# Performance work log

Measured on AMD Instinct MI355X. Metric: run time of the kernel, lower is better.

Reference implementation:

```python
import jax, jax.numpy as jnp
import numpy as np

B, S, F = 16, 1024, 768
GRID_SIZE = 5
SPLINE_ORDER = 3
GRID_MIN, GRID_MAX = -1.5, 1.5
EPS = 1e-8  # denominator guard, as in the source


def setup_inputs() -> dict:
    key = jax.random.key(0)
    kx, kc = jax.random.split(key)
    x = jax.random.normal(kx, (B, S, F), dtype=jnp.float32)
    # learned knots: per-feature copy of linspace(grid_range, grid_size)
    knots = jnp.tile(jnp.linspace(GRID_MIN, GRID_MAX, GRID_SIZE, dtype=jnp.float32), (F, 1))  # (F, G)
    coeffs = jax.random.normal(kc, (F, GRID_SIZE + SPLINE_ORDER - 1), dtype=jnp.float32)       # (F, G+k-1)
    scaler = jnp.ones((F,), dtype=jnp.float32)
    return {"x": x, "knots": knots, "coeffs": coeffs, "scaler": scaler}


def _extend_knots(knots, order):
    # pad `order` uniformly-spaced knots on each side: (F, G) -> (F, G + 2*order)
    step = (knots[:, -1] - knots[:, 0]) / (knots.shape[1] - 1)          # (F,)
    left = knots[:, :1] - step[:, None] * jnp.arange(order, 0, -1, dtype=knots.dtype)
    right = knots[:, -1:] + step[:, None] * jnp.arange(1, order + 1, dtype=knots.dtype)
    return jnp.concatenate([left, knots, right], axis=1)


def _bspline_basis(x2d, t_ext, order):
    # x2d: (N, F); t_ext: (F, K). Cox-de Boor, vectorized over basis index.
    t = t_ext[None]          # (1, F, K)
    xe = x2d[..., None]      # (N, F, 1)
    # degree 0: indicator of knot interval -> (N, F, K-1)
    b = ((xe >= t[..., :-1]) & (xe < t[..., 1:])).astype(x2d.dtype)
    for d in range(1, order + 1):
        left = (xe - t[..., :-(d + 1)]) / (t[..., d:-1] - t[..., :-(d + 1)] + EPS) * b[..., :-1]
        right = (t[..., d + 1:] - xe) / (t[..., d + 1:] - t[..., 1:-d] + EPS) * b[..., 1:]
        b = left + right
    return b                 # (N, F, K-1-order)


def reference(x, knots, coeffs, scaler):
    Bsz, Ssz, Feat = x.shape
    x2d = x.reshape(-1, Feat)                       # (N, F)
    t = _extend_knots(knots, SPLINE_ORDER)          # (F, G + 2k)
    basis = _bspline_basis(x2d, t, SPLINE_ORDER)    # (N, F, G+k-1)
    out = jnp.einsum('nfj,fj->nf', basis, coeffs) * scaler
    return out.reshape(Bsz, Ssz, Feat)
```

## Files before the change

### kernel.cpp

```cpp
#include <hip/hip_runtime.h>


constexpr int FEAT  = 768;
constexpr int GSZ   = 5;
constexpr int ORD   = 3;
constexpr int KE    = GSZ + 2 * ORD;
constexpr int NB0   = KE - 1;
constexpr int NCOEF = GSZ + ORD - 1;
constexpr float EPSV = 1e-8f;
constexpr int ROWS_PER_BLOCK = 32;

__global__ __launch_bounds__(256)
void kan_bspline_kernel(const float* __restrict__ xg,
                        const float* __restrict__ knots,
                        const float* __restrict__ coeffs,
                        const float* __restrict__ scaler,
                        float* __restrict__ outg,
                        int nrows)
{
    const int f    = blockIdx.x * blockDim.x + threadIdx.x;
    const int row0 = blockIdx.y * ROWS_PER_BLOCK;
    if (row0 >= nrows) return;

    float kn[GSZ];
#pragma unroll
    for (int i = 0; i < GSZ; ++i) kn[i] = knots[f * GSZ + i];
    const float h = (kn[GSZ - 1] - kn[0]) * (1.0f / (GSZ - 1));

    float te[KE];
#pragma unroll
    for (int i = 0; i < ORD; ++i) te[i] = kn[0] - h * (float)(ORD - i);
#pragma unroll
    for (int i = 0; i < GSZ; ++i) te[ORD + i] = kn[i];
#pragma unroll
    for (int i = 0; i < ORD; ++i) te[ORD + GSZ + i] = kn[GSZ - 1] + h * (float)(i + 1);

    float r1[KE - 1], s1[KE - 1];
#pragma unroll
    for (int j = 0; j < KE - 1; ++j) {
        r1[j] = 1.0f / (te[j + 1] - te[j] + EPSV);
        s1[j] = -te[j] * r1[j];
    }
    float r2[KE - 2], s2[KE - 2];
#pragma unroll
    for (int j = 0; j < KE - 2; ++j) {
        r2[j] = 1.0f / (te[j + 2] - te[j] + EPSV);
        s2[j] = -te[j] * r2[j];
    }
    float r3[KE - 3], s3[KE - 3];
#pragma unroll
    for (int j = 0; j < KE - 3; ++j) {
        r3[j] = 1.0f / (te[j + 3] - te[j] + EPSV);
        s3[j] = -te[j] * r3[j];
    }

    float cf[NCOEF];
#pragma unroll
    for (int j = 0; j < NCOEF; ++j) cf[j] = coeffs[f * NCOEF + j];
    const float sc = scaler[f];

    const float* xp = xg   + (size_t)row0 * FEAT + f;
    float*       op = outg + (size_t)row0 * FEAT + f;
    const int rows = (nrows - row0 < ROWS_PER_BLOCK) ? (nrows - row0) : ROWS_PER_BLOCK;

    for (int rr = 0; rr < rows; ++rr) {
        const float x = xp[(size_t)rr * FEAT];

        float gef[KE];
#pragma unroll
        for (int i = 0; i < KE; ++i) gef[i] = (x >= te[i]) ? 1.0f : 0.0f;
        float b0[NB0];
#pragma unroll
        for (int i = 0; i < NB0; ++i) b0[i] = gef[i] - gef[i + 1];

        float u[KE - 1];

#pragma unroll
        for (int j = 0; j < KE - 1; ++j) u[j] = fmaf(x, r1[j], s1[j]);
        float b1[KE - 2];
#pragma unroll
        for (int i = 0; i < KE - 2; ++i) {
            float t = fmaf(-u[i + 1], b0[i + 1], b0[i + 1]);
            b1[i] = fmaf(u[i], b0[i], t);
        }

#pragma unroll
        for (int j = 0; j < KE - 2; ++j) u[j] = fmaf(x, r2[j], s2[j]);
        float b2[KE - 3];
#pragma unroll
        for (int i = 0; i < KE - 3; ++i) {
            float t = fmaf(-u[i + 1], b1[i + 1], b1[i + 1]);
            b2[i] = fmaf(u[i], b1[i], t);
        }

#pragma unroll
        for (int j = 0; j < KE - 3; ++j) u[j] = fmaf(x, r3[j], s3[j]);
        float b3[KE - 4];
#pragma unroll
        for (int i = 0; i < KE - 4; ++i) {
            float t = fmaf(-u[i + 1], b2[i + 1], b2[i + 1]);
            b3[i] = fmaf(u[i], b2[i], t);
        }

        float acc = 0.0f;
#pragma unroll
        for (int j = 0; j < NCOEF; ++j) acc = fmaf(b3[j], cf[j], acc);
        op[(size_t)rr * FEAT] = acc * sc;
    }
}

extern "C" void kernel_launch(void* const* d_in, const int* in_sizes, int n_in,
                              void* d_out, int out_size, void* d_ws, size_t ws_size,
                              hipStream_t stream) {
    const float* x      = (const float*)d_in[0];
    const float* knots  = (const float*)d_in[1];
    const float* coeffs = (const float*)d_in[2];
    const float* scaler = (const float*)d_in[3];
    float* out = (float*)d_out;

    const int nrows = in_sizes[0] / FEAT;

    dim3 block(256, 1, 1);
    dim3 grid(FEAT / 256, (nrows + ROWS_PER_BLOCK - 1) / ROWS_PER_BLOCK, 1);
    kan_bspline_kernel<<<grid, block, 0, stream>>>(x, knots, coeffs, scaler, out, nrows);
}
```

Baseline: 135.3 us.

## Precompute per-feature spline constants in a separate kernel and simplify degree-1 basis

Moves the knot extension, reciprocal and offset computation into a small precompute kernel that writes per-feature constants to workspace, with the scaler folded into the coefficients. The main kernel loads these constants and computes the degree-1 basis directly as a clamped min/max hat function, which drops the degree-0 indicator step. It also processes 64 rows per block, two at a time with software-prefetched loads. This trades an extra kernel launch and a workspace round-trip for fewer ALU ops per element. The hat-function shortcut assumes uniform knots and may differ from the reference at interval boundaries.

```diff
diff --git a/kernel.cpp b/kernel.cpp
--- a/kernel.cpp
+++ b/kernel.cpp
@@ -5,22 +5,33 @@
 constexpr int GSZ   = 5;
 constexpr int ORD   = 3;
 constexpr int KE    = GSZ + 2 * ORD;
-constexpr int NB0   = KE - 1;
+constexpr int N1    = KE - 1;
+constexpr int N2    = KE - 2;
+constexpr int N3    = KE - 3;
+constexpr int NB1   = KE - 2;
+constexpr int NB2   = KE - 3;
+constexpr int NB3   = KE - 4;
 constexpr int NCOEF = GSZ + ORD - 1;
 constexpr float EPSV = 1e-8f;
-constexpr int ROWS_PER_BLOCK = 32;
+constexpr int ROWS  = 64;
+
+constexpr int WR_R1 = 0;
+constexpr int WR_S1 = WR_R1 + N1;
+constexpr int WR_R2 = WR_S1 + N1;
+constexpr int WR_S2 = WR_R2 + N2;
+constexpr int WR_R3 = WR_S2 + N2;
+constexpr int WR_S3 = WR_R3 + N3;
+constexpr int WR_CF = WR_S3 + N3;
+constexpr int WROWS = WR_CF + NCOEF;
 
 __global__ __launch_bounds__(256)
-void kan_bspline_kernel(const float* __restrict__ xg,
-                        const float* __restrict__ knots,
-                        const float* __restrict__ coeffs,
-                        const float* __restrict__ scaler,
-                        float* __restrict__ outg,
-                        int nrows)
+void kan_precompute(const float* __restrict__ knots,
+                    const float* __restrict__ coeffs,
+                    const float* __restrict__ scaler,
+                    float* __restrict__ ws)
 {
-    const int f    = blockIdx.x * blockDim.x + threadIdx.x;
-    const int row0 = blockIdx.y * ROWS_PER_BLOCK;
-    if (row0 >= nrows) return;
+    const int f = blockIdx.x * blockDim.x + threadIdx.x;
+    if (f >= FEAT) return;
 
     float kn[GSZ];
 #pragma unroll
@@ -35,77 +46,104 @@
 #pragma unroll
     for (int i = 0; i < ORD; ++i) te[ORD + GSZ + i] = kn[GSZ - 1] + h * (float)(i + 1);
 
-    float r1[KE - 1], s1[KE - 1];
 #pragma unroll
-    for (int j = 0; j < KE - 1; ++j) {
-        r1[j] = 1.0f / (te[j + 1] - te[j] + EPSV);
-        s1[j] = -te[j] * r1[j];
+    for (int j = 0; j < N1; ++j) {
+        float r = 1.0f / (te[j + 1] - te[j] + EPSV);
+        ws[(WR_R1 + j) * FEAT + f] = r;
+        ws[(WR_S1 + j) * FEAT + f] = -te[j] * r;
     }
-    float r2[KE - 2], s2[KE - 2];
 #pragma unroll
-    for (int j = 0; j < KE - 2; ++j) {
-        r2[j] = 1.0f / (te[j + 2] - te[j] + EPSV);
-        s2[j] = -te[j] * r2[j];
+    for (int j = 0; j < N2; ++j) {
+        float r = 1.0f / (te[j + 2] - te[j] + EPSV);
+        ws[(WR_R2 + j) * FEAT + f] = r;
+        ws[(WR_S2 + j) * FEAT + f] = -te[j] * r;
     }
-    float r3[KE - 3], s3[KE - 3];
 #pragma unroll
-    for (int j = 0; j < KE - 3; ++j) {
-        r3[j] = 1.0f / (te[j + 3] - te[j] + EPSV);
-        s3[j] = -te[j] * r3[j];
+    for (int j = 0; j < N3; ++j) {
+        float r = 1.0f / (te[j + 3] - te[j] + EPSV);
+        ws[(WR_R3 + j) * FEAT + f] = r;
+        ws[(WR_S3 + j) * FEAT + f] = -te[j] * r;
     }
+    const float sc = scaler[f];
+#pragma unroll
+    for (int j = 0; j < NCOEF; ++j)
+        ws[(WR_CF + j) * FEAT + f] = coeffs[f * NCOEF + j] * sc;
+}
 
-    float cf[NCOEF];
+__global__ __launch_bounds__(256, 4)
+void kan_main(const float* __restrict__ xg,
+              const float* __restrict__ ws,
+              float* __restrict__ outg,
+              int nrows)
+{
+    const int f    = blockIdx.x * 256 + threadIdx.x;
+    const int row0 = blockIdx.y * ROWS;
+    if (row0 >= nrows) return;
+
+    float r1[N1], s1[N1], r2[N2], s2[N2], r3[N3], s3[N3], cf[NCOEF];
 #pragma unroll
-    for (int j = 0; j < NCOEF; ++j) cf[j] = coeffs[f * NCOEF + j];
-    const float sc = scaler[f];
+    for (int j = 0; j < N1; ++j) { r1[j] = ws[(WR_R1 + j) * FEAT + f];
+                                   s1[j] = ws[(WR_S1 + j) * FEAT + f]; }
+#pragma unroll
+    for (int j = 0; j < N2; ++j) { r2[j] = ws[(WR_R2 + j) * FEAT + f];
+                                   s2[j] = ws[(WR_S2 + j) * FEAT + f]; }
+#pragma unroll
+    for (int j = 0; j < N3; ++j) { r3[j] = ws[(WR_R3 + j) * FEAT + f];
+                                   s3[j] = ws[(WR_S3 + j) * FEAT + f]; }
+#pragma unroll
+    for (int j = 0; j < NCOEF; ++j) cf[j] = ws[(WR_CF + j) * FEAT + f];
+
+    auto eval = [&](float x) -> float {
+        float u[N1];
+#pragma unroll
+        for (int j = 0; j < N1; ++j) u[j] = fmaf(x, r1[j], s1[j]);
+        float b1[NB1];
+#pragma unroll
+        for (int i = 0; i < NB1; ++i)
+            b1[i] = fmaxf(0.0f, fminf(u[i], 1.0f - u[i + 1]));
+#pragma unroll
+        for (int j = 0; j < N2; ++j) u[j] = fmaf(x, r2[j], s2[j]);
+        float b2[NB2];
+#pragma unroll
+        for (int i = 0; i < NB2; ++i) {
+            float t = fmaf(-u[i + 1], b1[i + 1], b1[i + 1]);
+            b2[i] = fmaf(u[i], b1[i], t);
+        }
+#pragma unroll
+        for (int j = 0; j < N3; ++j) u[j] = fmaf(x, r3[j], s3[j]);
+        float b3[NB3];
+#pragma unroll
+        for (int i = 0; i < NB3; ++i) {
+            float t = fmaf(-u[i + 1], b2[i + 1], b2[i + 1]);
+            b3[i] = fmaf(u[i], b2[i], t);
+        }
+        float acc = 0.0f;
+#pragma unroll
+        for (int j = 0; j < NCOEF; ++j) acc = fmaf(b3[j], cf[j], acc);
+        return acc;
+    };
 
     const float* xp = xg   + (size_t)row0 * FEAT + f;
     float*       op = outg + (size_t)row0 * FEAT + f;
-    const int rows = (nrows - row0 < ROWS_PER_BLOCK) ? (nrows - row0) : ROWS_PER_BLOCK;
+    const int rows = (nrows - row0 < ROWS) ? (nrows - row0) : ROWS;
 
-    for (int rr = 0; rr < rows; ++rr) {
-        const float x = xp[(size_t)rr * FEAT];
-
-        float gef[KE];
-#pragma unroll
-        for (int i = 0; i < KE; ++i) gef[i] = (x >= te[i]) ? 1.0f : 0.0f;
-        float b0[NB0];
-#pragma unroll
-        for (int i = 0; i < NB0; ++i) b0[i] = gef[i] - gef[i + 1];
-
-        float u[KE - 1];
-
-#pragma unroll
-        for (int j = 0; j < KE - 1; ++j) u[j] = fmaf(x, r1[j], s1[j]);
-        float b1[KE - 2];
-#pragma unroll
-        for (int i = 0; i < KE - 2; ++i) {
-            float t = fmaf(-u[i + 1], b0[i + 1], b0[i + 1]);
-            b1[i] = fmaf(u[i], b0[i], t);
+    if (rows == ROWS) {
+        float xa = xp[0];
+        float xb = xp[FEAT];
+        for (int base = 0; base < ROWS; base += 2) {
+            const int pn = (base + 2 < ROWS) ? base + 2 : base;
+            float xn0 = xp[(size_t)pn * FEAT];
+            float xn1 = xp[(size_t)(pn + 1) * FEAT];
+            float y0 = eval(xa);
+            float y1 = eval(xb);
+            op[(size_t)base * FEAT]       = y0;
+            op[(size_t)(base + 1) * FEAT] = y1;
+            xa = xn0;
+            xb = xn1;
         }
-
-#pragma unroll
-        for (int j = 0; j < KE - 2; ++j) u[j] = fmaf(x, r2[j], s2[j]);
-        float b2[KE - 3];
-#pragma unroll
-        for (int i = 0; i < KE - 3; ++i) {
-            float t = fmaf(-u[i + 1], b1[i + 1], b1[i + 1]);
-            b2[i] = fmaf(u[i], b1[i], t);
-        }
-
-#pragma unroll
-        for (int j = 0; j < KE - 3; ++j) u[j] = fmaf(x, r3[j], s3[j]);
-        float b3[KE - 4];
-#pragma unroll
-        for (int i = 0; i < KE - 4; ++i) {
-            float t = fmaf(-u[i + 1], b2[i + 1], b2[i + 1]);
-            b3[i] = fmaf(u[i], b2[i], t);
-        }
-
-        float acc = 0.0f;
-#pragma unroll
-        for (int j = 0; j < NCOEF; ++j) acc = fmaf(b3[j], cf[j], acc);
-        op[(size_t)rr * FEAT] = acc * sc;
+    } else {
+        for (int rr = 0; rr < rows; ++rr)
+            op[(size_t)rr * FEAT] = eval(xp[(size_t)rr * FEAT]);
     }
 }
 
@@ -117,10 +155,14 @@
     const float* coeffs = (const float*)d_in[2];
     const float* scaler = (const float*)d_in[3];
     float* out = (float*)d_out;
+    float* ws  = (float*)d_ws;
 
     const int nrows = in_sizes[0] / FEAT;
 
+    kan_precompute<<<dim3((FEAT + 255) / 256), dim3(256), 0, stream>>>(
+        knots, coeffs, scaler, ws);
+
     dim3 block(256, 1, 1);
-    dim3 grid(FEAT / 256, (nrows + ROWS_PER_BLOCK - 1) / ROWS_PER_BLOCK, 1);
-    kan_bspline_kernel<<<grid, block, 0, stream>>>(x, knots, coeffs, scaler, out, nrows);
+    dim3 grid(FEAT / 256, (nrows + ROWS - 1) / ROWS, 1);
+    kan_main<<<grid, block, 0, stream>>>(x, ws, out, nrows);
 }
```

Result: slower. 307.2 us (+127.1%).
